# Performance work log

Measured on AMD Instinct MI355X. Metric: run time of the kernel, lower is better.

The kernel has to match this reference:

```python
import jax, jax.numpy as jnp
import numpy as np

K = 3            # opt.kernel_size
L = 2            # opt.map_layers
MARGIN = 0.1     # opt.global_margin
NEG_NUM = 3      # opt.neg_num
FIRST_PAD = (K - 1) * L // 2


def conv2d(x, w, pad):
    return jax.lax.conv_general_dilated(x, w, (1, 1), [(pad, pad), (pad, pad)],
                                        dimension_numbers=('NCHW', 'OIHW', 'NCHW'))


def mask2weight(m, pad):
    ker = jnp.ones((1, 1, K, K), jnp.float32)
    w = conv2d(m.astype(jnp.float32)[None, None], ker, pad)[0, 0]
    return jnp.where(w > 0, 1.0 / jnp.maximum(w, 1.0), 0.0)


def setup_inputs():
    key = jax.random.key(0)
    ks = jax.random.split(key, 10)
    b, c, d, t, Lw = 8, 128, 64, 64, 20
    P = d * t
    v_map = jax.random.normal(ks[0], (b, c, d, t), jnp.float32)
    words = jax.random.normal(ks[1], (b, Lw, c), jnp.float32)
    w_masks = jnp.ones((b, Lw), jnp.float32)
    v_mask = jnp.triu(jnp.ones((d, t), jnp.float32))
    valid_num = jax.random.randint(ks[2], (b,), d // 2, t + 1)
    iou_maps = jax.random.uniform(ks[3], (P, P), jnp.float32)
    lam = jnp.float32(0.5)
    sc = np.float32(1.0 / np.sqrt(c * K * K))
    sp = np.float32(1.0 / np.sqrt(c))
    Wc0 = jax.random.normal(ks[4], (c, c, K, K), jnp.float32) * sc
    Wc1 = jax.random.normal(ks[5], (c, c, K, K), jnp.float32) * sc
    bc0 = jnp.zeros((c,), jnp.float32)
    bc1 = jnp.zeros((c,), jnp.float32)
    Wp0 = jax.random.normal(ks[6], (c, c), jnp.float32) * sp
    bp0 = jnp.zeros((c,), jnp.float32)
    Wp1 = jax.random.normal(ks[7], (c, c), jnp.float32) * sp
    bp1 = jnp.zeros((c,), jnp.float32)
    W2d = jax.random.normal(ks[8], (1, c, 1, 1), jnp.float32) * sp
    b2d = jnp.zeros((1,), jnp.float32)
    return dict(v_map=v_map, words=words, w_masks=w_masks, v_mask=v_mask,
                valid_num=valid_num, iou_maps=iou_maps, lam=lam,
                Wc0=Wc0, bc0=bc0, Wc1=Wc1, bc1=bc1,
                Wp0=Wp0, bp0=bp0, Wp1=Wp1, bp1=bp1, W2d=W2d, b2d=b2d)


def _forward(v_map, words, w_masks, v_mask, valid_num, iou_maps, lam,
             Wc0, bc0, Wc1, bc1, Wp0, bp0, Wp1, bp1, W2d, b2d):
    b, c, d, t = v_map.shape
    P = d * t
    neg_inf = jnp.float32(-jnp.inf)
    # mask-normalized conv weights, recomputed from v_mask as in __init__
    weight0 = mask2weight(v_mask, FIRST_PAD)          # [d+2*FIRST_PAD-K+1, ...]
    weight1 = mask2weight(weight0 > 0, 0)             # back to [d, t]
    cols = jnp.arange(t)
    vm3 = (v_mask[None] > 0) & (cols[None, None, :] < valid_num[:, None, None])  # [b,d,t]

    def per_sentence(i):
        wm = w_masks[i]
        pooled = (words[i] * wm[:, None]).sum(0) / jnp.maximum(wm.sum(), 1.0)  # [c]
        g0 = jnp.tanh(pooled @ Wp0 + bp0)
        g1 = jnp.tanh(pooled @ Wp1 + bp1)
        # layer 1 (padded), layer 2 (unpadded) -- word-gated, mask-normalized convs
        x = conv2d(v_map, Wc0, FIRST_PAD) + bc0[None, :, None, None]
        x = jax.nn.relu(x * weight0[None, None] * g0[None, :, None, None])
        x = conv2d(x, Wc1, 0) + bc1[None, :, None, None]
        x = jax.nn.relu(x * weight1[None, None] * g1[None, :, None, None])
        s = jax.nn.sigmoid(conv2d(x, W2d, 0)[:, 0] + b2d[0])  # [b, d, t]
        s = jnp.where(vm3, s, neg_inf)
        pmap_i = s[i]
        sflat = s.reshape(b, P)
        pos = sflat.max(1)          # per-video score for sentence i -> [b]
        si = sflat[i]
        pos_idx = jnp.argmax(si)
        iou_row = iou_maps[pos_idx]  # IoU of best proposal vs all proposals
        negs = jnp.where((iou_row < lam) & jnp.isfinite(si), si, neg_inf)
        hard = negs.max()           # hardest NMS-suppressed negative proposal
        neg_loss = jax.nn.relu(MARGIN + hard - pos[i])
        return pos, pmap_i, neg_loss

    scores, positive_map, neg_losses = jax.lax.map(per_sentence, jnp.arange(b))
    negative_loss = neg_losses.mean()
    diagonal = jnp.diag(scores)[:, None]
    cost_s = jax.nn.relu(MARGIN + scores - diagonal)      # sentence -> video
    cost_im = jax.nn.relu(MARGIN + scores - diagonal.T)   # video -> sentence
    eye = jnp.eye(b, dtype=bool)
    cost_s = jnp.where(eye, 0.0, cost_s)
    cost_im = jnp.where(eye, 0.0, cost_im)
    # max_violation: keep NEG_NUM hardest negatives (sort desc == top_k)
    cost_s = jax.lax.top_k(cost_s, NEG_NUM)[0]
    cost_im = jax.lax.top_k(cost_im.T, NEG_NUM)[0]
    loss = cost_s.sum() / b + cost_im.sum() / b + negative_loss
    return loss, positive_map


def reference(v_map, words, w_masks, v_mask, valid_num, iou_maps, lam,
              Wc0, bc0, Wc1, bc1, Wp0, bp0, Wp1, bp1, W2d, b2d):
    return _forward(v_map, words, w_masks, v_mask, valid_num, iou_maps, lam,
                    Wc0, bc0, Wc1, bc1, Wp0, bp0, Wp1, bp1, W2d, b2d)
```

## Files before the change

### kernel.cpp

```cpp
#include <hip/hip_runtime.h>
#include <hip/hip_bf16.h>
#include <math.h>

#define BB 8
#define CC 128
#define DD 64
#define TT 64
#define PP 4096
#define H1 66
#define LW 20
#define MARGINF 0.1f
#define NEG_SENTINEL -1.0e30f

#define Y0_OFF   0
#define VT_OFF   2230272
#define BP0_OFF  4327424
#define NL_OFF   4401152
#define W0_OFF   4479236
#define W1_OFF   4483592
#define G0_OFF   4487688
#define G1_OFF   4488712
#define S_OFF    4489736
#define SCP_OFF  4522504
#define BP1S_OFF 4522632

typedef __attribute__((ext_vector_type(8))) short bf16x8;
typedef __attribute__((ext_vector_type(4))) float f32x4;

#define ASTR 44

__device__ __forceinline__ unsigned f2bf(float f) {
  union { float f; unsigned u; } v; v.f = f;
  unsigned r = v.u + 0x7fffu + ((v.u >> 16) & 1u);
  return r >> 16;
}
__device__ __forceinline__ float bf2f(unsigned hw) {
  union { unsigned u; float f; } v; v.u = hw << 16;
  return v.f;
}
__device__ __forceinline__ unsigned cvt_bf(float x) {
  __hip_bfloat16 h = __float2bfloat16(x);
  union { __hip_bfloat16 h; unsigned short u; } cv; cv.h = h;
  return (unsigned)cv.u;
}

__device__ __forceinline__ unsigned selbf(unsigned d, unsigned W) {
  unsigned diff = (d ^ W) & 0x80008000u;
  unsigned full = (diff >> 15) * 0xFFFFu;
  return d & ~full;
}

__global__ __launch_bounds__(256) void setup_kernel(
    const float* __restrict__ vmap, const float* __restrict__ v_mask,
    const float* __restrict__ Wc0,
    const float* __restrict__ words, const float* __restrict__ w_masks,
    const float* __restrict__ Wp0, const float* __restrict__ bp0,
    const float* __restrict__ Wp1, const float* __restrict__ bp1,
    float* __restrict__ ws)
{
  __shared__ float smem[64 * 129];
  int bid = blockIdx.x;
  int t = threadIdx.x;

  if (bid < 576) {
    unsigned short* dst = (unsigned short*)(ws + BP0_OFF);
    int idx = bid * 256 + t;
    int j    = idx & 7;
    int lane = (idx >> 3) & 63;
    int cog  = (idx >> 9) & 7;
    int cic  = (idx >> 12) & 3;
    int kk   = idx >> 14;
    int co = cog * 16 + (lane & 15);
    int ci = cic * 32 + (lane >> 4) * 8 + j;
    dst[idx] = (unsigned short)f2bf(Wc0[(co * CC + ci) * 9 + kk]);
  } else if (bid < 1088) {
    unsigned short* vT = (unsigned short*)(ws + VT_OFF);
    int b = bid - 576;
    int n = b & 7, y = b >> 3;
    int x = t & 63, c4 = t >> 6;
    for (int rep = 0; rep < 32; ++rep) {
      int ci = rep * 4 + c4;
      smem[x * 129 + ci] = vmap[(((size_t)n * CC + ci) * DD + y) * TT + x];
    }
    __syncthreads();
    for (int rep = 0; rep < 16; ++rep) {
      int v = t + rep * 256;
      int xx = v >> 6, cip = v & 63;
      float a = smem[xx * 129 + cip * 2];
      float b2 = smem[xx * 129 + cip * 2 + 1];
      unsigned pk = f2bf(a) | (f2bf(b2) << 16);
      *(unsigned*)&vT[(((size_t)(n * DD + y) * TT + xx)) * CC + cip * 2] = pk;
    }
  } else if (bid == 1088) {
    if (t < 128) ((unsigned*)(ws + SCP_OFF))[t] = 0u;
    float* w0 = ws + W0_OFF;
    float* w1 = ws + W1_OFF;
    for (int idx = t; idx < H1 * H1; idx += 256) {
      int y = idx / H1, x = idx % H1;
      float cnt = 0.f;
      for (int ky = 0; ky < 3; ++ky)
        for (int kx = 0; kx < 3; ++kx) {
          int iy = y + ky - 2, ix = x + kx - 2;
          if (iy >= 0 && iy < DD && ix >= 0 && ix < TT) cnt += v_mask[iy * TT + ix];
        }
      w0[idx] = (cnt > 0.f) ? 1.f / fmaxf(cnt, 1.f) : 0.f;
    }
    __syncthreads();
    for (int idx = t; idx < DD * TT; idx += 256) {
      int y = idx / TT, x = idx % TT;
      float cnt = 0.f;
      for (int ky = 0; ky < 3; ++ky)
        for (int kx = 0; kx < 3; ++kx)
          cnt += (w0[(y + ky) * H1 + (x + kx)] > 0.f) ? 1.f : 0.f;
      w1[idx] = (cnt > 0.f) ? 1.f / fmaxf(cnt, 1.f) : 0.f;
    }
  } else {
    int i = bid - 1089;
    if (t < CC) {
      float wsum = 0.f, acc = 0.f;
      for (int l = 0; l < LW; ++l) {
        float wm = w_masks[i * LW + l];
        wsum += wm;
        acc += words[(i * LW + l) * CC + t] * wm;
      }
      smem[t] = acc / fmaxf(wsum, 1.f);
    }
    __syncthreads();
    {
      int c = t & 127;
      const float* Wp = (t < 128) ? Wp0 : Wp1;
      const float* bp = (t < 128) ? bp0 : bp1;
      float a = bp[c];
      for (int k = 0; k < CC; ++k) a += smem[k] * Wp[k * CC + c];
      float g = tanhf(a);
      float* gout = ws + ((t < 128) ? G0_OFF : G1_OFF);
      gout[i * CC + c] = g;
    }
  }
}

__global__ __launch_bounds__(256, 3) void conv1_mfma(
    const float* __restrict__ bc0, const float* __restrict__ Wc1,
    float* __restrict__ ws)
{
  __shared__ unsigned short Alds[3 * 68 * ASTR];

  int t = threadIdx.x;
  int id = blockIdx.x;

  if (id >= 1056) {
    float* smem = (float*)Alds;
    for (int v = t; v < 8 * CC; v += 256) smem[v] = ws[G0_OFF + v];
    __syncthreads();
    int idx = (id - 1056) * 256 + t;
    int j    = idx & 7;
    int lane = (idx >> 3) & 63;
    int cog  = (idx >> 9) & 7;
    int cic  = (idx >> 12) & 3;
    int kk   = idx >> 14;
    int co = cog * 16 + (lane & 15);
    int ci = cic * 32 + (lane >> 4) * 8 + j;
    float wv = Wc1[(co * CC + ci) * 9 + kk];
    unsigned short* dst = (unsigned short*)(ws + BP1S_OFF);
#pragma unroll
    for (int si = 0; si < 8; ++si)
      dst[si * 147456 + idx] = (unsigned short)f2bf(wv * smem[si * CC + ci]);
    return;
  }

  const unsigned short* vT = (const unsigned short*)(ws + VT_OFF);
  const unsigned short* Bp = (const unsigned short*)(ws + BP0_OFF);
  const float* w0arr = ws + W0_OFF;
  unsigned short* y0w = (unsigned short*)(ws + Y0_OFF);

  int n  = id & 7;
  int ch = (id >> 3) & 1;
  int r0 = id >> 4;
  int lane = t & 63, w = t >> 6;
  int l15 = lane & 15, l4 = lane >> 4;
  int s = ch * 4 + w;
  int co0 = s * 16;

  f32x4 acc[5];
#pragma unroll
  for (int mf = 0; mf < 5; ++mf) acc[mf] = (f32x4){0.f, 0.f, 0.f, 0.f};

  for (int cic = 0; cic < 4; ++cic) {
    __syncthreads();
    for (int u = t; u < 816; u += 256) {
      int cig = u & 3, rest = u >> 2;
      int col = rest % 68, r = rest / 68;
      int iy = r0 - 2 + r, ix = col - 2;
      uint4 val = {0u, 0u, 0u, 0u};
      if (iy >= 0 && iy < DD && ix >= 0 && ix < TT)
        val = *(const uint4*)&vT[(((size_t)(n * DD + iy) * TT + ix)) * CC + cic * 32 + cig * 8];
      *(uint4*)&Alds[(r * 68 + col) * ASTR + cig * 8] = val;
    }
    __syncthreads();
    __builtin_amdgcn_s_setprio(1);
#pragma unroll
    for (int kk = 0; kk < 9; ++kk) {
      int ky = kk / 3, kx = kk % 3;
      bf16x8 af[5], bfr;
#pragma unroll
      for (int mf = 0; mf < 5; ++mf) {
        int c = mf * 16 + l15;
        int cc = c > 65 ? 65 : c;
        af[mf] = *(const bf16x8*)&Alds[(ky * 68 + cc + kx) * ASTR + l4 * 8];
      }
      bfr = *(const bf16x8*)&Bp[(((kk * 4 + cic) * 8 + s) * 64 + lane) * 8];
#pragma unroll
      for (int mf = 0; mf < 5; ++mf)
        acc[mf] = __builtin_amdgcn_mfma_f32_16x16x32_bf16(af[mf], bfr, acc[mf], 0, 0, 0);
    }
    __builtin_amdgcn_s_setprio(0);
  }

  int y = r0;
  {
    int co = co0 + l15;
    float bcv = bc0[co];
#pragma unroll
    for (int mf = 0; mf < 5; ++mf)
#pragma unroll
      for (int rg = 0; rg < 4; ++rg) {
        int c = mf * 16 + l4 * 4 + rg;
        if (c < H1) {
          float v = (acc[mf][rg] + bcv) * w0arr[y * H1 + c];
          y0w[((size_t)(n * H1 + y) * H1 + c) * CC + co] = (unsigned short)cvt_bf(v);
        }
      }
  }
}

__global__ __launch_bounds__(256, 3) void conv2_mfma(
    const float* __restrict__ bc1, const float* __restrict__ W2d,
    const float* __restrict__ b2d, const float* __restrict__ v_mask,
    const int* __restrict__ valid_num, float* __restrict__ ws,
    float* __restrict__ out)
{
  const unsigned short* y0w = (const unsigned short*)(ws + Y0_OFF);
  const float* w1m = ws + W1_OFF;
  const float* g0 = ws + G0_OFF;
  const float* g1 = ws + G1_OFF;
  unsigned long long* scp = (unsigned long long*)(ws + SCP_OFF);

  __shared__ unsigned short Alds[4 * 66 * ASTR];
  __shared__ unsigned msk[16][4];
  __shared__ float redl[2][2][64];
  __shared__ unsigned long long kred[2];

  int t = threadIdx.x;
  int r0 = blockIdx.x;
  int i = blockIdx.y & 7, n = blockIdx.y >> 3;
  int lane = t & 63, w = t >> 6;
  int wr = w >> 1, wc = w & 1;
  int l15 = lane & 15, l4 = lane >> 4;

  const unsigned short* Bp = (const unsigned short*)(ws + BP1S_OFF) + (size_t)i * 147456;

  if (t < 16) {
    int ch = t * 8;
    msk[t][0] = (g0[i * CC + ch + 0] > 0.f ? 0u : 0x8000u) | (g0[i * CC + ch + 1] > 0.f ? 0u : 0x80000000u);
    msk[t][1] = (g0[i * CC + ch + 2] > 0.f ? 0u : 0x8000u) | (g0[i * CC + ch + 3] > 0.f ? 0u : 0x80000000u);
    msk[t][2] = (g0[i * CC + ch + 4] > 0.f ? 0u : 0x8000u) | (g0[i * CC + ch + 5] > 0.f ? 0u : 0x80000000u);
    msk[t][3] = (g0[i * CC + ch + 6] > 0.f ? 0u : 0x8000u) | (g0[i * CC + ch + 7] > 0.f ? 0u : 0x80000000u);
  }

  f32x4 acc[4][4];
#pragma unroll
  for (int mf = 0; mf < 4; ++mf)
#pragma unroll
    for (int nf = 0; nf < 4; ++nf) acc[mf][nf] = (f32x4){0.f, 0.f, 0.f, 0.f};

  for (int cic = 0; cic < 4; ++cic) {
    __syncthreads();
    {
      uint4 mv = *(const uint4*)&msk[(cic << 2) | (t & 3)][0];
      for (int u = t; u < 1056; u += 256) {
        int cig = u & 3, cr = u >> 2;
        int col = cr % 66, row = cr / 66;
        const unsigned short* src = y0w
            + ((size_t)((n * H1 + r0 * 2 + row) * H1 + col)) * CC + cic * 32 + cig * 8;
        uint4 raw = *(const uint4*)src;
        uint4 pk;
        pk.x = selbf(raw.x, mv.x);
        pk.y = selbf(raw.y, mv.y);
        pk.z = selbf(raw.z, mv.z);
        pk.w = selbf(raw.w, mv.w);
        *(uint4*)&Alds[(row * 66 + col) * ASTR + cig * 8] = pk;
      }
    }
    __syncthreads();
    __builtin_amdgcn_s_setprio(1);
#pragma unroll
    for (int kk = 0; kk < 9; ++kk) {
      int ky = kk / 3, kx = kk % 3;
      bf16x8 af[4], bfr[4];
#pragma unroll
      for (int mf = 0; mf < 4; ++mf) {
        int row = wr + ky;
        int col = mf * 16 + l15 + kx;
        af[mf] = *(const bf16x8*)&Alds[(row * 66 + col) * ASTR + l4 * 8];
      }
#pragma unroll
      for (int nf = 0; nf < 4; ++nf)
        bfr[nf] = *(const bf16x8*)&Bp[(((kk * 4 + cic) * 8 + wc * 4 + nf) * 64 + lane) * 8];
#pragma unroll
      for (int mf = 0; mf < 4; ++mf)
#pragma unroll
        for (int nf = 0; nf < 4; ++nf)
          acc[mf][nf] = __builtin_amdgcn_mfma_f32_16x16x32_bf16(af[mf], bfr[nf], acc[mf][nf], 0, 0, 0);
    }
    __builtin_amdgcn_s_setprio(0);
  }

  float part[4][4];
#pragma unroll
  for (int mf = 0; mf < 4; ++mf)
#pragma unroll
    for (int rg = 0; rg < 4; ++rg) part[mf][rg] = 0.f;
#pragma unroll
  for (int nf = 0; nf < 4; ++nf) {
    int co = wc * 64 + nf * 16 + l15;
    float bcv = bc1[co];
    float gv = g1[i * CC + co];
    float wv = W2d[co];
#pragma unroll
    for (int mf = 0; mf < 4; ++mf)
#pragma unroll
      for (int rg = 0; rg < 4; ++rg) {
        float z = (acc[mf][nf][rg] + bcv) * gv;
        part[mf][rg] += fmaxf(z, 0.f) * wv;
      }
  }
#pragma unroll
  for (int mask = 1; mask < 16; mask <<= 1)
#pragma unroll
    for (int mf = 0; mf < 4; ++mf)
#pragma unroll
      for (int rg = 0; rg < 4; ++rg)
        part[mf][rg] += __shfl_xor(part[mf][rg], mask, 64);
  if (l15 == 0) {
#pragma unroll
    for (int mf = 0; mf < 4; ++mf)
#pragma unroll
      for (int rg = 0; rg < 4; ++rg)
        redl[wc][wr][mf * 16 + l4 * 4 + rg] = part[mf][rg];
  }
  __syncthreads();
  if (t < 128) {
    int row = t >> 6, col = t & 63;
    int rowg = r0 * 2 + row;
    float v = redl[0][row][col] + redl[1][row][col];
    float logit = w1m[rowg * TT + col] * v + b2d[0];
    float sig = 1.f / (1.f + expf(-logit));
    bool m = (v_mask[rowg * TT + col] > 0.f) && (col < valid_num[n]);
    int p = rowg * TT + col;
    if (i == n) {
      ws[S_OFF + i * PP + p] = m ? sig : -INFINITY;
      out[1 + i * PP + p] = m ? sig : NEG_SENTINEL;
    }
    unsigned long long key = 0ull;
    if (m) key = ((unsigned long long)__float_as_uint(sig) << 32)
                 | (unsigned long long)(0xFFFFFFFFu - (unsigned)p);
#pragma unroll
    for (int mk = 1; mk < 64; mk <<= 1) {
      unsigned lo = __shfl_xor((unsigned)key, mk, 64);
      unsigned hi = __shfl_xor((unsigned)(key >> 32), mk, 64);
      unsigned long long o = ((unsigned long long)hi << 32) | lo;
      if (o > key) key = o;
    }
    if (lane == 0) kred[w] = key;
  }
  __syncthreads();
  if (t == 0) {
    unsigned long long k = kred[0];
    if (kred[1] > k) k = kred[1];
    if (k) atomicMax(&scp[i * 8 + n], k);
  }
}

__global__ __launch_bounds__(256) void mine_kernel(
    const float* __restrict__ iou_maps, const float* __restrict__ lam,
    float* __restrict__ ws)
{
  __shared__ float wred[4];
  int i = blockIdx.x;
  int t = threadIdx.x, lane = t & 63, w = t >> 6;
  const unsigned long long* scp = (const unsigned long long*)(ws + SCP_OFF);

  unsigned long long dk = scp[i * 9];
  float diag_sc = __uint_as_float((unsigned)(dk >> 32));
  int pidx = (int)(0xFFFFFFFFu - (unsigned)(dk & 0xFFFFFFFFu));
  float lamv = lam[0];
  const float* row = iou_maps + (size_t)pidx * PP;
  const float* si = ws + S_OFF + (size_t)i * PP;
  float hv = -INFINITY;
  for (int p = t; p < PP; p += 256) {
    float v = si[p];
    if (row[p] < lamv && isfinite(v)) hv = fmaxf(hv, v);
  }
#pragma unroll
  for (int m = 1; m < 64; m <<= 1) hv = fmaxf(hv, __shfl_xor(hv, m, 64));
  if (lane == 0) wred[w] = hv;
  __syncthreads();
  if (t == 0) {
    float h = fmaxf(fmaxf(wred[0], wred[1]), fmaxf(wred[2], wred[3]));
    ws[NL_OFF + i] = fmaxf(0.f, MARGINF + h - diag_sc);
  }
}

__global__ __launch_bounds__(64) void loss_kernel(
    float* __restrict__ ws, float* __restrict__ out)
{
  __shared__ float scsh[64];
  int lane = threadIdx.x;
  const unsigned long long* scp = (const unsigned long long*)(ws + SCP_OFF);
  scsh[lane] = __uint_as_float((unsigned)(scp[lane] >> 32));
  __syncthreads();

  float partial = 0.f;
  if (lane < 16) {
    int r = lane & 7;
    bool im = lane >= 8;
    float diag = scsh[r * 8 + r];
    float v[8];
#pragma unroll
    for (int j = 0; j < 8; ++j) {
      float scv = im ? scsh[j * 8 + r] : scsh[r * 8 + j];
      float h = fmaxf(0.f, MARGINF + scv - diag);
      v[j] = (j == r) ? 0.f : h;
    }
#define CE(a, b) { float mx = fmaxf(v[a], v[b]); float mn = fminf(v[a], v[b]); v[a] = mx; v[b] = mn; }
    CE(0,1) CE(2,3) CE(4,5) CE(6,7)
    CE(0,2) CE(1,3) CE(4,6) CE(5,7)
    CE(1,2) CE(5,6)
    CE(0,4) CE(1,5) CE(2,6) CE(3,7)
    CE(2,4) CE(3,5)
    CE(1,2) CE(3,4) CE(5,6)
#undef CE
    partial = v[0] + v[1] + v[2];
  } else if (lane >= 16 && lane < 24) {
    partial = ws[NL_OFF + lane - 16];
  }
#pragma unroll
  for (int m = 1; m < 64; m <<= 1) partial += __shfl_xor(partial, m, 64);
  if (lane == 0) out[0] = partial * 0.125f;
}

extern "C" void kernel_launch(void* const* d_in, const int* in_sizes, int n_in,
                              void* d_out, int out_size, void* d_ws, size_t ws_size,
                              hipStream_t stream)
{
  const float* v_map     = (const float*)d_in[0];
  const float* words     = (const float*)d_in[1];
  const float* w_masks   = (const float*)d_in[2];
  const float* v_mask    = (const float*)d_in[3];
  const int*   valid_num = (const int*)d_in[4];
  const float* iou_maps  = (const float*)d_in[5];
  const float* lam       = (const float*)d_in[6];
  const float* Wc0 = (const float*)d_in[7];
  const float* bc0 = (const float*)d_in[8];
  const float* Wc1 = (const float*)d_in[9];
  const float* bc1 = (const float*)d_in[10];
  const float* Wp0 = (const float*)d_in[11];
  const float* bp0 = (const float*)d_in[12];
  const float* Wp1 = (const float*)d_in[13];
  const float* bp1 = (const float*)d_in[14];
  const float* W2d = (const float*)d_in[15];
  const float* b2d = (const float*)d_in[16];
  float* ws  = (float*)d_ws;
  float* out = (float*)d_out;

  hipLaunchKernelGGL(setup_kernel, dim3(1097), dim3(256), 0, stream,
                     v_map, v_mask, Wc0, words, w_masks, Wp0, bp0, Wp1, bp1, ws);
  hipLaunchKernelGGL(conv1_mfma, dim3(1632), dim3(256), 0, stream, bc0, Wc1, ws);
  hipLaunchKernelGGL(conv2_mfma, dim3(32, 64), dim3(256), 0, stream,
                     bc1, W2d, b2d, v_mask, valid_num, ws, out);
  hipLaunchKernelGGL(mine_kernel, dim3(8), dim3(256), 0, stream, iou_maps, lam, ws);
  hipLaunchKernelGGL(loss_kernel, dim3(1), dim3(64), 0, stream, ws, out);
}
```

Baseline: 133.8 us.

## Reuse conv2 input tile across four sentences per block with in-register masking

Each conv2 block now loads the full 4-row by 66-column by 128-channel y0 tile into LDS once and loops over four sentences, instead of reloading a 32-channel slice per sentence. The per-sentence gating mask is applied on the fly when fragments are read from LDS rather than at staging time, so the same staged data serves all four sentences. The grid shrinks fourfold and the occupancy hint drops from 3 to 2 blocks per CU to fit the larger LDS footprint. Per-block parallelism and overlap of loads with compute go down, and each LDS read now carries extra select work.

```diff
diff --git a/kernel.cpp b/kernel.cpp
--- a/kernel.cpp
+++ b/kernel.cpp
@@ -28,6 +28,8 @@
 typedef __attribute__((ext_vector_type(4))) float f32x4;
 
 #define ASTR 44
+#define A2STR 36
+#define A2PL  (4 * 66 * A2STR)
 
 __device__ __forceinline__ unsigned f2bf(float f) {
   union { float f; unsigned u; } v; v.f = f;
@@ -233,7 +235,7 @@
   }
 }
 
-__global__ __launch_bounds__(256, 3) void conv2_mfma(
+__global__ __launch_bounds__(256, 2) void conv2_mfma(
     const float* __restrict__ bc1, const float* __restrict__ W2d,
     const float* __restrict__ b2d, const float* __restrict__ v_mask,
     const int* __restrict__ valid_num, float* __restrict__ ws,
@@ -245,139 +247,143 @@
   const float* g1 = ws + G1_OFF;
   unsigned long long* scp = (unsigned long long*)(ws + SCP_OFF);
 
-  __shared__ unsigned short Alds[4 * 66 * ASTR];
-  __shared__ unsigned msk[16][4];
+  __shared__ unsigned short Alds[4 * A2PL];
+  __shared__ unsigned msk[4][16][4];
   __shared__ float redl[2][2][64];
   __shared__ unsigned long long kred[2];
 
   int t = threadIdx.x;
   int r0 = blockIdx.x;
-  int i = blockIdx.y & 7, n = blockIdx.y >> 3;
+  int ip = blockIdx.y & 1, n = blockIdx.y >> 1;
   int lane = t & 63, w = t >> 6;
   int wr = w >> 1, wc = w & 1;
   int l15 = lane & 15, l4 = lane >> 4;
 
-  const unsigned short* Bp = (const unsigned short*)(ws + BP1S_OFF) + (size_t)i * 147456;
-
-  if (t < 16) {
-    int ch = t * 8;
-    msk[t][0] = (g0[i * CC + ch + 0] > 0.f ? 0u : 0x8000u) | (g0[i * CC + ch + 1] > 0.f ? 0u : 0x80000000u);
-    msk[t][1] = (g0[i * CC + ch + 2] > 0.f ? 0u : 0x8000u) | (g0[i * CC + ch + 3] > 0.f ? 0u : 0x80000000u);
-    msk[t][2] = (g0[i * CC + ch + 4] > 0.f ? 0u : 0x8000u) | (g0[i * CC + ch + 5] > 0.f ? 0u : 0x80000000u);
-    msk[t][3] = (g0[i * CC + ch + 6] > 0.f ? 0u : 0x8000u) | (g0[i * CC + ch + 7] > 0.f ? 0u : 0x80000000u);
-  }
-
-  f32x4 acc[4][4];
-#pragma unroll
-  for (int mf = 0; mf < 4; ++mf)
-#pragma unroll
-    for (int nf = 0; nf < 4; ++nf) acc[mf][nf] = (f32x4){0.f, 0.f, 0.f, 0.f};
-
-  for (int cic = 0; cic < 4; ++cic) {
-    __syncthreads();
-    {
-      uint4 mv = *(const uint4*)&msk[(cic << 2) | (t & 3)][0];
-      for (int u = t; u < 1056; u += 256) {
-        int cig = u & 3, cr = u >> 2;
-        int col = cr % 66, row = cr / 66;
-        const unsigned short* src = y0w
-            + ((size_t)((n * H1 + r0 * 2 + row) * H1 + col)) * CC + cic * 32 + cig * 8;
-        uint4 raw = *(const uint4*)src;
-        uint4 pk;
-        pk.x = selbf(raw.x, mv.x);
-        pk.y = selbf(raw.y, mv.y);
-        pk.z = selbf(raw.z, mv.z);
-        pk.w = selbf(raw.w, mv.w);
-        *(uint4*)&Alds[(row * 66 + col) * ASTR + cig * 8] = pk;
-      }
-    }
-    __syncthreads();
+  if (t < 64) {
+    int ii = t >> 4, g = t & 15;
+    int i = ip * 4 + ii;
+    int ch = g * 8;
+    msk[ii][g][0] = (g0[i * CC + ch + 0] > 0.f ? 0u : 0x8000u) | (g0[i * CC + ch + 1] > 0.f ? 0u : 0x80000000u);
+    msk[ii][g][1] = (g0[i * CC + ch + 2] > 0.f ? 0u : 0x8000u) | (g0[i * CC + ch + 3] > 0.f ? 0u : 0x80000000u);
+    msk[ii][g][2] = (g0[i * CC + ch + 4] > 0.f ? 0u : 0x8000u) | (g0[i * CC + ch + 5] > 0.f ? 0u : 0x80000000u);
+    msk[ii][g][3] = (g0[i * CC + ch + 6] > 0.f ? 0u : 0x8000u) | (g0[i * CC + ch + 7] > 0.f ? 0u : 0x80000000u);
+  }
+
+  for (int u = t; u < 4224; u += 256) {
+    int cig = u & 3, cic = (u >> 2) & 3, cr = u >> 4;
+    int col = cr % 66, row = cr / 66;
+    uint4 raw = *(const uint4*)&y0w[((size_t)((n * H1 + r0 * 2 + row) * H1 + col)) * CC
+                                    + cic * 32 + cig * 8];
+    *(uint4*)&Alds[cic * A2PL + (row * 66 + col) * A2STR + cig * 8] = raw;
+  }
+  __syncthreads();
+
+#pragma unroll 1
+  for (int ii = 0; ii < 4; ++ii) {
+    int i = ip * 4 + ii;
+    const unsigned short* Bp = (const unsigned short*)(ws + BP1S_OFF) + (size_t)i * 147456;
+
+    f32x4 acc[4][4];
+#pragma unroll
+    for (int mf = 0; mf < 4; ++mf)
+#pragma unroll
+      for (int nf = 0; nf < 4; ++nf) acc[mf][nf] = (f32x4){0.f, 0.f, 0.f, 0.f};
+
     __builtin_amdgcn_s_setprio(1);
-#pragma unroll
-    for (int kk = 0; kk < 9; ++kk) {
-      int ky = kk / 3, kx = kk % 3;
-      bf16x8 af[4], bfr[4];
-#pragma unroll
-      for (int mf = 0; mf < 4; ++mf) {
-        int row = wr + ky;
-        int col = mf * 16 + l15 + kx;
-        af[mf] = *(const bf16x8*)&Alds[(row * 66 + col) * ASTR + l4 * 8];
-      }
-#pragma unroll
-      for (int nf = 0; nf < 4; ++nf)
-        bfr[nf] = *(const bf16x8*)&Bp[(((kk * 4 + cic) * 8 + wc * 4 + nf) * 64 + lane) * 8];
+    for (int cic = 0; cic < 4; ++cic) {
+      uint4 mv = *(const uint4*)&msk[ii][(cic << 2) | l4][0];
+#pragma unroll
+      for (int kk = 0; kk < 9; ++kk) {
+        int ky = kk / 3, kx = kk % 3;
+        bf16x8 af[4], bfr[4];
+#pragma unroll
+        for (int mf = 0; mf < 4; ++mf) {
+          int row = wr + ky;
+          int col = mf * 16 + l15 + kx;
+          uint4 raw = *(const uint4*)&Alds[cic * A2PL + (row * 66 + col) * A2STR + l4 * 8];
+          union { uint4 u; bf16x8 v; } cv_;
+          cv_.u.x = selbf(raw.x, mv.x);
+          cv_.u.y = selbf(raw.y, mv.y);
+          cv_.u.z = selbf(raw.z, mv.z);
+          cv_.u.w = selbf(raw.w, mv.w);
+          af[mf] = cv_.v;
+        }
+#pragma unroll
+        for (int nf = 0; nf < 4; ++nf)
+          bfr[nf] = *(const bf16x8*)&Bp[(((kk * 4 + cic) * 8 + wc * 4 + nf) * 64 + lane) * 8];
+#pragma unroll
+        for (int mf = 0; mf < 4; ++mf)
+#pragma unroll
+          for (int nf = 0; nf < 4; ++nf)
+            acc[mf][nf] = __builtin_amdgcn_mfma_f32_16x16x32_bf16(af[mf], bfr[nf], acc[mf][nf], 0, 0, 0);
+      }
+    }
+    __builtin_amdgcn_s_setprio(0);
+
+    float part[4][4];
+#pragma unroll
+    for (int mf = 0; mf < 4; ++mf)
+#pragma unroll
+      for (int rg = 0; rg < 4; ++rg) part[mf][rg] = 0.f;
+#pragma unroll
+    for (int nf = 0; nf < 4; ++nf) {
+      int co = wc * 64 + nf * 16 + l15;
+      float bcv = bc1[co];
+      float gv = g1[i * CC + co];
+      float wv = W2d[co];
 #pragma unroll
       for (int mf = 0; mf < 4; ++mf)
 #pragma unroll
-        for (int nf = 0; nf < 4; ++nf)
-          acc[mf][nf] = __builtin_amdgcn_mfma_f32_16x16x32_bf16(af[mf], bfr[nf], acc[mf][nf], 0, 0, 0);
-    }
-    __builtin_amdgcn_s_setprio(0);
-  }
-
-  float part[4][4];
-#pragma unroll
-  for (int mf = 0; mf < 4; ++mf)
-#pragma unroll
-    for (int rg = 0; rg < 4; ++rg) part[mf][rg] = 0.f;
-#pragma unroll
-  for (int nf = 0; nf < 4; ++nf) {
-    int co = wc * 64 + nf * 16 + l15;
-    float bcv = bc1[co];
-    float gv = g1[i * CC + co];
-    float wv = W2d[co];
-#pragma unroll
-    for (int mf = 0; mf < 4; ++mf)
-#pragma unroll
-      for (int rg = 0; rg < 4; ++rg) {
-        float z = (acc[mf][nf][rg] + bcv) * gv;
-        part[mf][rg] += fmaxf(z, 0.f) * wv;
-      }
-  }
-#pragma unroll
-  for (int mask = 1; mask < 16; mask <<= 1)
-#pragma unroll
-    for (int mf = 0; mf < 4; ++mf)
-#pragma unroll
-      for (int rg = 0; rg < 4; ++rg)
-        part[mf][rg] += __shfl_xor(part[mf][rg], mask, 64);
-  if (l15 == 0) {
-#pragma unroll
-    for (int mf = 0; mf < 4; ++mf)
-#pragma unroll
-      for (int rg = 0; rg < 4; ++rg)
-        redl[wc][wr][mf * 16 + l4 * 4 + rg] = part[mf][rg];
-  }
-  __syncthreads();
-  if (t < 128) {
-    int row = t >> 6, col = t & 63;
-    int rowg = r0 * 2 + row;
-    float v = redl[0][row][col] + redl[1][row][col];
-    float logit = w1m[rowg * TT + col] * v + b2d[0];
-    float sig = 1.f / (1.f + expf(-logit));
-    bool m = (v_mask[rowg * TT + col] > 0.f) && (col < valid_num[n]);
-    int p = rowg * TT + col;
-    if (i == n) {
-      ws[S_OFF + i * PP + p] = m ? sig : -INFINITY;
-      out[1 + i * PP + p] = m ? sig : NEG_SENTINEL;
-    }
-    unsigned long long key = 0ull;
-    if (m) key = ((unsigned long long)__float_as_uint(sig) << 32)
-                 | (unsigned long long)(0xFFFFFFFFu - (unsigned)p);
-#pragma unroll
-    for (int mk = 1; mk < 64; mk <<= 1) {
-      unsigned lo = __shfl_xor((unsigned)key, mk, 64);
-      unsigned hi = __shfl_xor((unsigned)(key >> 32), mk, 64);
-      unsigned long long o = ((unsigned long long)hi << 32) | lo;
-      if (o > key) key = o;
-    }
-    if (lane == 0) kred[w] = key;
-  }
-  __syncthreads();
-  if (t == 0) {
-    unsigned long long k = kred[0];
-    if (kred[1] > k) k = kred[1];
-    if (k) atomicMax(&scp[i * 8 + n], k);
+        for (int rg = 0; rg < 4; ++rg) {
+          float z = (acc[mf][nf][rg] + bcv) * gv;
+          part[mf][rg] += fmaxf(z, 0.f) * wv;
+        }
+    }
+#pragma unroll
+    for (int mask = 1; mask < 16; mask <<= 1)
+#pragma unroll
+      for (int mf = 0; mf < 4; ++mf)
+#pragma unroll
+        for (int rg = 0; rg < 4; ++rg)
+          part[mf][rg] += __shfl_xor(part[mf][rg], mask, 64);
+    if (l15 == 0) {
+#pragma unroll
+      for (int mf = 0; mf < 4; ++mf)
+#pragma unroll
+        for (int rg = 0; rg < 4; ++rg)
+          redl[wc][wr][mf * 16 + l4 * 4 + rg] = part[mf][rg];
+    }
+    __syncthreads();
+    if (t < 128) {
+      int row = t >> 6, col = t & 63;
+      int rowg = r0 * 2 + row;
+      float v = redl[0][row][col] + redl[1][row][col];
+      float logit = w1m[rowg * TT + col] * v + b2d[0];
+      float sig = 1.f / (1.f + expf(-logit));
+      bool m = (v_mask[rowg * TT + col] > 0.f) && (col < valid_num[n]);
+      int p = rowg * TT + col;
+      if (i == n) {
+        ws[S_OFF + i * PP + p] = m ? sig : -INFINITY;
+        out[1 + i * PP + p] = m ? sig : NEG_SENTINEL;
+      }
+      unsigned long long key = 0ull;
+      if (m) key = ((unsigned long long)__float_as_uint(sig) << 32)
+                   | (unsigned long long)(0xFFFFFFFFu - (unsigned)p);
+#pragma unroll
+      for (int mk = 1; mk < 64; mk <<= 1) {
+        unsigned lo = __shfl_xor((unsigned)key, mk, 64);
+        unsigned hi = __shfl_xor((unsigned)(key >> 32), mk, 64);
+        unsigned long long o = ((unsigned long long)hi << 32) | lo;
+        if (o > key) key = o;
+      }
+      if (lane == 0) kred[w] = key;
+    }
+    __syncthreads();
+    if (t == 0) {
+      unsigned long long k = kred[0];
+      if (kred[1] > k) k = kred[1];
+      if (k) atomicMax(&scp[i * 8 + n], k);
+    }
   }
 }
 
@@ -476,7 +482,7 @@
   hipLaunchKernelGGL(setup_kernel, dim3(1097), dim3(256), 0, stream,
                      v_map, v_mask, Wc0, words, w_masks, Wp0, bp0, Wp1, bp1, ws);
   hipLaunchKernelGGL(conv1_mfma, dim3(1632), dim3(256), 0, stream, bc0, Wc1, ws);
-  hipLaunchKernelGGL(conv2_mfma, dim3(32, 64), dim3(256), 0, stream,
+  hipLaunchKernelGGL(conv2_mfma, dim3(32, 16), dim3(256), 0, stream,
                      bc1, W2d, b2d, v_mask, valid_num, ws, out);
   hipLaunchKernelGGL(mine_kernel, dim3(8), dim3(256), 0, stream, iou_maps, lam, ws);
   hipLaunchKernelGGL(loss_kernel, dim3(1), dim3(64), 0, stream, ws, out);
```

Measured after the change: 172.1 us. +28.7%, slower.

## Fuse mining and loss kernels into conv2 via last-block atomic counters

Applied to the files above, without the earlier changes.

Removes the separate mine_kernel and loss_kernel launches. Per-sentence atomic counters, zeroed in setup, let the last conv2 block for each sentence run the hard-negative mining. A second counter lets the last mining block compute the final loss. This saves two kernel launches and their gaps, at the cost of threadfences, atomics and a serial tail inside the final conv2 blocks.

```diff
diff --git a/kernel.cpp b/kernel.cpp
--- a/kernel.cpp
+++ b/kernel.cpp
@@ -93,6 +93,7 @@
     }
   } else if (bid == 1088) {
     if (t < 128) ((unsigned*)(ws + SCP_OFF))[t] = 0u;
+    if (t >= 128 && t < 137) ((unsigned*)(ws + NL_OFF + 8))[t - 128] = 0u;
     float* w0 = ws + W0_OFF;
     float* w1 = ws + W1_OFF;
     for (int idx = t; idx < H1 * H1; idx += 256) {
@@ -236,19 +237,22 @@
 __global__ __launch_bounds__(256, 3) void conv2_mfma(
     const float* __restrict__ bc1, const float* __restrict__ W2d,
     const float* __restrict__ b2d, const float* __restrict__ v_mask,
-    const int* __restrict__ valid_num, float* __restrict__ ws,
-    float* __restrict__ out)
+    const int* __restrict__ valid_num,
+    const float* __restrict__ iou_maps, const float* __restrict__ lam,
+    float* __restrict__ ws, float* __restrict__ out)
 {
   const unsigned short* y0w = (const unsigned short*)(ws + Y0_OFF);
   const float* w1m = ws + W1_OFF;
   const float* g0 = ws + G0_OFF;
   const float* g1 = ws + G1_OFF;
   unsigned long long* scp = (unsigned long long*)(ws + SCP_OFF);
+  unsigned* cnt = (unsigned*)(ws + NL_OFF + 8);
 
   __shared__ unsigned short Alds[4 * 66 * ASTR];
   __shared__ unsigned msk[16][4];
   __shared__ float redl[2][2][64];
   __shared__ unsigned long long kred[2];
+  __shared__ unsigned lflag, lflag2;
 
   int t = threadIdx.x;
   int r0 = blockIdx.x;
@@ -378,75 +382,74 @@
     unsigned long long k = kred[0];
     if (kred[1] > k) k = kred[1];
     if (k) atomicMax(&scp[i * 8 + n], k);
-  }
-}
-
-__global__ __launch_bounds__(256) void mine_kernel(
-    const float* __restrict__ iou_maps, const float* __restrict__ lam,
-    float* __restrict__ ws)
-{
-  __shared__ float wred[4];
-  int i = blockIdx.x;
-  int t = threadIdx.x, lane = t & 63, w = t >> 6;
-  const unsigned long long* scp = (const unsigned long long*)(ws + SCP_OFF);
-
-  unsigned long long dk = scp[i * 9];
-  float diag_sc = __uint_as_float((unsigned)(dk >> 32));
-  int pidx = (int)(0xFFFFFFFFu - (unsigned)(dk & 0xFFFFFFFFu));
-  float lamv = lam[0];
-  const float* row = iou_maps + (size_t)pidx * PP;
-  const float* si = ws + S_OFF + (size_t)i * PP;
-  float hv = -INFINITY;
-  for (int p = t; p < PP; p += 256) {
-    float v = si[p];
-    if (row[p] < lamv && isfinite(v)) hv = fmaxf(hv, v);
-  }
-#pragma unroll
-  for (int m = 1; m < 64; m <<= 1) hv = fmaxf(hv, __shfl_xor(hv, m, 64));
-  if (lane == 0) wred[w] = hv;
+    __threadfence();
+    unsigned old = atomicAdd(&cnt[i], 1u);
+    lflag = (old == 255u) ? 1u : 0u;
+  }
   __syncthreads();
-  if (t == 0) {
-    float h = fmaxf(fmaxf(wred[0], wred[1]), fmaxf(wred[2], wred[3]));
-    ws[NL_OFF + i] = fmaxf(0.f, MARGINF + h - diag_sc);
-  }
-}
-
-__global__ __launch_bounds__(64) void loss_kernel(
-    float* __restrict__ ws, float* __restrict__ out)
-{
-  __shared__ float scsh[64];
-  int lane = threadIdx.x;
-  const unsigned long long* scp = (const unsigned long long*)(ws + SCP_OFF);
-  scsh[lane] = __uint_as_float((unsigned)(scp[lane] >> 32));
-  __syncthreads();
-
-  float partial = 0.f;
-  if (lane < 16) {
-    int r = lane & 7;
-    bool im = lane >= 8;
-    float diag = scsh[r * 8 + r];
-    float v[8];
-#pragma unroll
-    for (int j = 0; j < 8; ++j) {
-      float scv = im ? scsh[j * 8 + r] : scsh[r * 8 + j];
-      float h = fmaxf(0.f, MARGINF + scv - diag);
-      v[j] = (j == r) ? 0.f : h;
-    }
+
+  if (lflag) {
+    __threadfence();
+    float* wred = &redl[0][0][0];
+    unsigned long long dk = scp[i * 9];
+    float diag_sc = __uint_as_float((unsigned)(dk >> 32));
+    int pidx = (int)(0xFFFFFFFFu - (unsigned)(dk & 0xFFFFFFFFu));
+    float lamv = lam[0];
+    const float* row = iou_maps + (size_t)pidx * PP;
+    const float* si = ws + S_OFF + (size_t)i * PP;
+    float hv = -INFINITY;
+    for (int p = t; p < PP; p += 256) {
+      float v = si[p];
+      if (row[p] < lamv && isfinite(v)) hv = fmaxf(hv, v);
+    }
+#pragma unroll
+    for (int m = 1; m < 64; m <<= 1) hv = fmaxf(hv, __shfl_xor(hv, m, 64));
+    if (lane == 0) wred[w] = hv;
+    __syncthreads();
+    if (t == 0) {
+      float h = fmaxf(fmaxf(wred[0], wred[1]), fmaxf(wred[2], wred[3]));
+      ws[NL_OFF + i] = fmaxf(0.f, MARGINF + h - diag_sc);
+      __threadfence();
+      unsigned o2 = atomicAdd(&cnt[8], 1u);
+      lflag2 = (o2 == 7u) ? 1u : 0u;
+    }
+    __syncthreads();
+    if (lflag2) {
+      __threadfence();
+      float* scsh = &redl[1][0][0];
+      if (t < 64) scsh[t] = __uint_as_float((unsigned)(scp[t] >> 32));
+      __syncthreads();
+      if (t < 64) {
+        float partial = 0.f;
+        if (lane < 16) {
+          int r = lane & 7;
+          bool im = lane >= 8;
+          float diag = scsh[r * 8 + r];
+          float v[8];
+#pragma unroll
+          for (int j = 0; j < 8; ++j) {
+            float scv = im ? scsh[j * 8 + r] : scsh[r * 8 + j];
+            float h = fmaxf(0.f, MARGINF + scv - diag);
+            v[j] = (j == r) ? 0.f : h;
+          }
 #define CE(a, b) { float mx = fmaxf(v[a], v[b]); float mn = fminf(v[a], v[b]); v[a] = mx; v[b] = mn; }
-    CE(0,1) CE(2,3) CE(4,5) CE(6,7)
-    CE(0,2) CE(1,3) CE(4,6) CE(5,7)
-    CE(1,2) CE(5,6)
-    CE(0,4) CE(1,5) CE(2,6) CE(3,7)
-    CE(2,4) CE(3,5)
-    CE(1,2) CE(3,4) CE(5,6)
+          CE(0,1) CE(2,3) CE(4,5) CE(6,7)
+          CE(0,2) CE(1,3) CE(4,6) CE(5,7)
+          CE(1,2) CE(5,6)
+          CE(0,4) CE(1,5) CE(2,6) CE(3,7)
+          CE(2,4) CE(3,5)
+          CE(1,2) CE(3,4) CE(5,6)
 #undef CE
-    partial = v[0] + v[1] + v[2];
-  } else if (lane >= 16 && lane < 24) {
-    partial = ws[NL_OFF + lane - 16];
-  }
-#pragma unroll
-  for (int m = 1; m < 64; m <<= 1) partial += __shfl_xor(partial, m, 64);
-  if (lane == 0) out[0] = partial * 0.125f;
+          partial = v[0] + v[1] + v[2];
+        } else if (lane >= 16 && lane < 24) {
+          partial = ws[NL_OFF + lane - 16];
+        }
+#pragma unroll
+        for (int m = 1; m < 64; m <<= 1) partial += __shfl_xor(partial, m, 64);
+        if (lane == 0) out[0] = partial * 0.125f;
+      }
+    }
+  }
 }
 
 extern "C" void kernel_launch(void* const* d_in, const int* in_sizes, int n_in,
@@ -477,7 +480,5 @@
                      v_map, v_mask, Wc0, words, w_masks, Wp0, bp0, Wp1, bp1, ws);
   hipLaunchKernelGGL(conv1_mfma, dim3(1632), dim3(256), 0, stream, bc0, Wc1, ws);
   hipLaunchKernelGGL(conv2_mfma, dim3(32, 64), dim3(256), 0, stream,
-                     bc1, W2d, b2d, v_mask, valid_num, ws, out);
-  hipLaunchKernelGGL(mine_kernel, dim3(8), dim3(256), 0, stream, iou_maps, lam, ws);
-  hipLaunchKernelGGL(loss_kernel, dim3(1), dim3(64), 0, stream, ws, out);
-}
+                     bc1, W2d, b2d, v_mask, valid_num, iou_maps, lam, ws, out);
+}
```

New measurement: 165.2 us. 1.24x slower.
